# Kernel tuning notes

Hardware: AMD Instinct MI355X
Metric: run time of the kernel (lower is better)

The kernel has to match this reference:

```python
import jax, jax.numpy as jnp
import numpy as np

KW = 3          # kernel_width
PAD = (KW - 1) // 2


def setup_inputs() -> dict:
    key = jax.random.key(0)
    ks = jax.random.split(key, 7)
    B, QL, KL, QS, KS = 16, 1024, 1024, 512, 512
    q = jax.random.normal(ks[0], (B, QL, QS), dtype=jnp.float32)
    k = jax.random.normal(ks[1], (B, KL, KS), dtype=jnp.float32)
    # torch Linear weights: [out_features, in_features]
    Wk = jax.random.normal(ks[2], (KS * KW, QS), dtype=jnp.float32) * (1.0 / np.sqrt(QS))
    bk = jax.random.normal(ks[3], (KS * KW,), dtype=jnp.float32) * 0.02
    Wb = jax.random.normal(ks[4], (1, QS), dtype=jnp.float32) * (1.0 / np.sqrt(QS))
    bb = jax.random.normal(ks[5], (1,), dtype=jnp.float32) * 0.02
    bias_b = jax.random.normal(ks[6], (1,), dtype=jnp.float32)
    return {"q": q, "k": k, "Wk": Wk, "bk": bk, "Wb": Wb, "bb": bb, "bias_b": bias_b}


def reference(q, k, Wk, bk, Wb, bb, bias_b):
    B, QL, QS = q.shape
    _, KL, KS = k.shape
    # per-query dynamic kernels: [B, QL, KS, KW]
    kernel = (jnp.einsum('biq,oq->bio', q, Wk) + bk).reshape(B, QL, KS, KW)
    # per-query scalar bias: [B, QL]
    bias = (jnp.einsum('biq,oq->bio', q, Wb) + bb)[..., 0]
    # banded multiply-accumulate, equivalent to grouped conv1d with groups=B
    k_pad = jnp.pad(k, ((0, 0), (PAD, PAD), (0, 0)))  # [B, KL+KW-1, KS]
    # windows[b, j, t, c] = k_pad[b, j+t, c]  -> [B, KL, KW, KS]
    windows = jnp.stack([k_pad[:, t:t + KL, :] for t in range(KW)], axis=2)
    scores = jnp.einsum('bict,bjtc->bij', kernel, windows)
    return scores + bias[:, :, None] + bias_b[0]
```

## Files before the change

kernel.cpp:

```cpp
#include <hip/hip_runtime.h>

typedef unsigned short ushort_t;
typedef unsigned int uint32;
typedef __bf16 bf16x8 __attribute__((ext_vector_type(8)));
typedef float f32x4 __attribute__((ext_vector_type(4)));
typedef float f4 __attribute__((ext_vector_type(4)));
typedef unsigned short us4 __attribute__((ext_vector_type(4)));


__device__ __forceinline__ ushort_t f2bf(float f) {
    uint32 u = __builtin_bit_cast(uint32, f);
    u = (u + 0x7fffu + ((u >> 16) & 1u)) >> 16;
    return (ushort_t)u;
}

#define FULL_BAR() do { __builtin_amdgcn_sched_barrier(0); __builtin_amdgcn_s_barrier(); __builtin_amdgcn_sched_barrier(0); } while (0)
#define HALF_BAR() do { __builtin_amdgcn_sched_barrier(0); __builtin_amdgcn_s_barrier(); } while (0)

__global__ __launch_bounds__(256) void prep_q(const float* __restrict__ q,
                                              const float* __restrict__ Wb,
                                              const float* __restrict__ bb,
                                              ushort_t* __restrict__ qb,
                                              float* __restrict__ biasw) {
    const int tid = threadIdx.x;
    const int lane = tid & 63, wid = tid >> 6;
    const int m = blockIdx.x * 4 + wid;
    const float* qrow = q + (size_t)m * 512;

    f4 v0 = *(const f4*)(qrow + lane * 4);
    f4 v1 = *(const f4*)(qrow + 256 + lane * 4);
    f4 w0 = *(const f4*)(Wb + lane * 4);
    f4 w1 = *(const f4*)(Wb + 256 + lane * 4);

    float dot = v0[0]*w0[0] + v0[1]*w0[1] + v0[2]*w0[2] + v0[3]*w0[3]
              + v1[0]*w1[0] + v1[1]*w1[1] + v1[2]*w1[2] + v1[3]*w1[3];

    us4 o0, o1;
    o0[0]=f2bf(v0[0]); o0[1]=f2bf(v0[1]); o0[2]=f2bf(v0[2]); o0[3]=f2bf(v0[3]);
    o1[0]=f2bf(v1[0]); o1[1]=f2bf(v1[1]); o1[2]=f2bf(v1[2]); o1[3]=f2bf(v1[3]);
    *(us4*)(qb + (size_t)m * 512 + lane * 4) = o0;
    *(us4*)(qb + (size_t)m * 512 + 256 + lane * 4) = o1;

    #pragma unroll
    for (int off = 32; off >= 1; off >>= 1) dot += __shfl_xor(dot, off);
    if (lane == 0) biasw[m] = dot + bb[0];
}

__global__ __launch_bounds__(256) void prep_k(const float* __restrict__ k,
                                              const float* __restrict__ Wk,
                                              const float* __restrict__ bk,
                                              ushort_t* __restrict__ kbp,
                                              ushort_t* __restrict__ wkb,
                                              float* __restrict__ bkp) {
    const int gid = blockIdx.x * 256 + threadIdx.x;
    if (gid < 1536) bkp[gid] = bk[(gid & 511) * 3 + (gid >> 9)];

    const int KG = (16 * 1024 * 512) / 4;
    const int PG = (16 * 2 * 512) / 4;

    if (gid < KG) {
        const int e = gid * 4;
        const int b = e >> 19;
        const int rem = e & ((1 << 19) - 1);
        const int row = rem >> 9, c = rem & 511;
        f4 v = *(const f4*)(k + e);
        us4 o; o[0]=f2bf(v[0]); o[1]=f2bf(v[1]); o[2]=f2bf(v[2]); o[3]=f2bf(v[3]);
        *(us4*)(kbp + ((size_t)b * 1026 + row + 1) * 512 + c) = o;
    } else if (gid < KG + PG) {
        const int p = gid - KG;
        const int b = p >> 8, off = p & 255;
        const int row = (off < 128) ? 0 : 1025;
        const int c = (off & 127) * 4;
        us4 z; z[0]=0; z[1]=0; z[2]=0; z[3]=0;
        *(us4*)(kbp + ((size_t)b * 1026 + row) * 512 + c) = z;
    } else {
        const int w = gid - KG - PG;
        const int n = w >> 7;
        const int c = (w & 127) * 4;
        const int o = (n & 511) * 3 + (n >> 9);
        f4 v = *(const f4*)(Wk + (size_t)o * 512 + c);
        us4 ov; ov[0]=f2bf(v[0]); ov[1]=f2bf(v[1]); ov[2]=f2bf(v[2]); ov[3]=f2bf(v[3]);
        *(us4*)(wkb + (size_t)n * 512 + c) = ov;
    }
}


__device__ __forceinline__ void stage16k(const char* base, int ld, char* dst, int tid) {
    #pragma unroll
    for (int inst = 0; inst < 2; ++inst) {
        const int idx = inst * 512 + tid;
        const int srow = idx >> 2;
        const int scol = ((idx & 3) ^ ((idx >> 3) & 3)) << 4;
        __builtin_amdgcn_global_load_lds(
            (const __attribute__((address_space(1))) void*)(base + (size_t)srow * (size_t)ld + scol),
            (__attribute__((address_space(3))) void*)(dst + (inst * 512 + (tid & ~63)) * 16),
            16, 0, 0);
    }
}

__global__ __launch_bounds__(512) void gemm1(const ushort_t* __restrict__ qb,
                                             const ushort_t* __restrict__ wkb,
                                             const float* __restrict__ bkp,
                                             ushort_t* __restrict__ coef) {
    __shared__ alignas(16) char lds[65536];
    const int tid = threadIdx.x;
    const int l = tid & 63, wid = tid >> 6;
    const int wr = wid >> 2, wc = wid & 3;
    int bid = blockIdx.x;
    bid = (bid & 7) * 48 + (bid >> 3);
    const int mt = bid & 63, nt = bid >> 6;
    const int mbase = mt * 256, nbase = nt * 256;

    const char* Ag = (const char*)(qb + (size_t)mbase * 512);
    const char* Bg = (const char*)(wkb + (size_t)nbase * 512);
    const int NT = 16;

    const int r15 = l & 15, q = l >> 4;
    const int laneoff = r15 * 64 + (((q ^ (r15 >> 1)) & 3) << 4);
    const int wrA = wr * 8192 + laneoff;
    const int wcB = wc * 4096 + laneoff;

    f32x4 acc[8][4];
    #pragma unroll
    for (int mi = 0; mi < 8; ++mi)
        #pragma unroll
        for (int ni = 0; ni < 4; ++ni)
            #pragma unroll
            for (int r = 0; r < 4; ++r) acc[mi][ni][r] = 0.f;

    stage16k(Ag, 1024, lds, tid);
    stage16k(Bg, 1024, lds + 16384, tid);
    stage16k(Ag + 64, 1024, lds + 32768, tid);
    asm volatile("s_waitcnt vmcnt(2)" ::: "memory");
    FULL_BAR();

    for (int t = 0; t < NT; ++t) {
        const int cur = (t & 1) << 15;
        const int nxt = cur ^ 32768;
        const char* lA = lds + cur;
        const char* lB = lds + cur + 16384;
        const int tn1 = (t + 1 < NT) ? t + 1 : NT - 1;
        const int tn2 = (t + 2 < NT) ? t + 2 : NT - 1;

        bf16x8 a[8], b0, b1;
        #pragma unroll
        for (int mi = 0; mi < 8; ++mi) a[mi] = *(const bf16x8*)(lA + wrA + mi * 1024);
        b0 = *(const bf16x8*)(lB + wcB);
        b1 = *(const bf16x8*)(lB + wcB + 1024);
        stage16k(Bg + tn1 * 64, 1024, lds + nxt + 16384, tid);
        FULL_BAR();
        __builtin_amdgcn_s_setprio(1);
        #pragma unroll
        for (int mi = 0; mi < 8; ++mi) {
            acc[mi][0] = __builtin_amdgcn_mfma_f32_16x16x32_bf16(a[mi], b0, acc[mi][0], 0, 0, 0);
            acc[mi][1] = __builtin_amdgcn_mfma_f32_16x16x32_bf16(a[mi], b1, acc[mi][1], 0, 0, 0);
        }
        __builtin_amdgcn_s_setprio(0);
        HALF_BAR();
        b0 = *(const bf16x8*)(lB + wcB + 2048);
        b1 = *(const bf16x8*)(lB + wcB + 3072);
        stage16k(Ag + tn2 * 64, 1024, lds + cur, tid);
        asm volatile("s_waitcnt vmcnt(2)" ::: "memory");
        FULL_BAR();
        __builtin_amdgcn_s_setprio(1);
        #pragma unroll
        for (int mi = 0; mi < 8; ++mi) {
            acc[mi][2] = __builtin_amdgcn_mfma_f32_16x16x32_bf16(a[mi], b0, acc[mi][2], 0, 0, 0);
            acc[mi][3] = __builtin_amdgcn_mfma_f32_16x16x32_bf16(a[mi], b1, acc[mi][3], 0, 0, 0);
        }
        __builtin_amdgcn_s_setprio(0);
        HALF_BAR();
    }

    #pragma unroll
    for (int ni = 0; ni < 4; ++ni) {
        const int ncol = nbase + wc * 64 + ni * 16 + r15;
        const float bkv = bkp[ncol];
        #pragma unroll
        for (int mi = 0; mi < 8; ++mi) {
            const int mrow0 = mbase + wr * 128 + mi * 16 + q * 4;
            #pragma unroll
            for (int r = 0; r < 4; ++r)
                coef[(size_t)(mrow0 + r) * 1536 + ncol] = f2bf(acc[mi][ni][r] + bkv);
        }
    }
}

__global__ __launch_bounds__(512) void gemm2(const ushort_t* __restrict__ coef,
                                             const ushort_t* __restrict__ kbp,
                                             const float* __restrict__ biasw,
                                             const float* __restrict__ bias_b,
                                             float* __restrict__ out) {
    __shared__ alignas(16) char lds[65536];
    const int tid = threadIdx.x;
    const int l = tid & 63, wid = tid >> 6;
    const int wr = wid >> 2, wc = wid & 3;
    int bid = blockIdx.x;
    bid = (bid & 7) * 32 + (bid >> 3);
    const int jt = bid & 3, it = (bid >> 2) & 3, b = bid >> 4;
    const int ibase = it * 256, jbase = jt * 256;

    const char* Ag = (const char*)(coef + ((size_t)b * 1024 + ibase) * 1536);
    const char* Bg = (const char*)(kbp + ((size_t)b * 1026 + jbase) * 512);
    const int NT = 48;

    const int r15 = l & 15, q = l >> 4;
    const int laneoff = r15 * 64 + (((q ^ (r15 >> 1)) & 3) << 4);
    const int wrA = wr * 8192 + laneoff;
    const int wcB = wc * 4096 + laneoff;

    f32x4 acc[8][4];
    #pragma unroll
    for (int mi = 0; mi < 8; ++mi)
        #pragma unroll
        for (int ni = 0; ni < 4; ++ni)
            #pragma unroll
            for (int r = 0; r < 4; ++r) acc[mi][ni][r] = 0.f;

    stage16k(Ag, 3072, lds, tid);
    stage16k(Bg, 1024, lds + 16384, tid);
    stage16k(Ag + 64, 3072, lds + 32768, tid);
    asm volatile("s_waitcnt vmcnt(2)" ::: "memory");
    FULL_BAR();

    for (int t = 0; t < NT; ++t) {
        const int cur = (t & 1) << 15;
        const int nxt = cur ^ 32768;
        const char* lA = lds + cur;
        const char* lB = lds + cur + 16384;
        const int tn1 = (t + 1 < NT) ? t + 1 : NT - 1;
        const int tn2 = (t + 2 < NT) ? t + 2 : NT - 1;

        bf16x8 a[8], b0, b1;
        #pragma unroll
        for (int mi = 0; mi < 8; ++mi) a[mi] = *(const bf16x8*)(lA + wrA + mi * 1024);
        b0 = *(const bf16x8*)(lB + wcB);
        b1 = *(const bf16x8*)(lB + wcB + 1024);
        stage16k(Bg + (tn1 >> 4) * 1024 + (tn1 & 15) * 64, 1024, lds + nxt + 16384, tid);
        FULL_BAR();
        __builtin_amdgcn_s_setprio(1);
        #pragma unroll
        for (int mi = 0; mi < 8; ++mi) {
            acc[mi][0] = __builtin_amdgcn_mfma_f32_16x16x32_bf16(a[mi], b0, acc[mi][0], 0, 0, 0);
            acc[mi][1] = __builtin_amdgcn_mfma_f32_16x16x32_bf16(a[mi], b1, acc[mi][1], 0, 0, 0);
        }
        __builtin_amdgcn_s_setprio(0);
        HALF_BAR();
        b0 = *(const bf16x8*)(lB + wcB + 2048);
        b1 = *(const bf16x8*)(lB + wcB + 3072);
        stage16k(Ag + tn2 * 64, 3072, lds + cur, tid);
        asm volatile("s_waitcnt vmcnt(2)" ::: "memory");
        FULL_BAR();
        __builtin_amdgcn_s_setprio(1);
        #pragma unroll
        for (int mi = 0; mi < 8; ++mi) {
            acc[mi][2] = __builtin_amdgcn_mfma_f32_16x16x32_bf16(a[mi], b0, acc[mi][2], 0, 0, 0);
            acc[mi][3] = __builtin_amdgcn_mfma_f32_16x16x32_bf16(a[mi], b1, acc[mi][3], 0, 0, 0);
        }
        __builtin_amdgcn_s_setprio(0);
        HALF_BAR();
    }

    const float bb0v = bias_b[0];
    #pragma unroll
    for (int mi = 0; mi < 8; ++mi) {
        const int irow0 = ibase + wr * 128 + mi * 16 + q * 4;
        #pragma unroll
        for (int r = 0; r < 4; ++r) {
            const float bv = biasw[b * 1024 + irow0 + r] + bb0v;
            #pragma unroll
            for (int ni = 0; ni < 4; ++ni) {
                const int jcol = jbase + wc * 64 + ni * 16 + r15;
                out[((size_t)b << 20) + (size_t)(irow0 + r) * 1024 + jcol] = acc[mi][ni][r] + bv;
            }
        }
    }
}

extern "C" void kernel_launch(void* const* d_in, const int* in_sizes, int n_in,
                              void* d_out, int out_size, void* d_ws, size_t ws_size,
                              hipStream_t stream) {
    const float* q      = (const float*)d_in[0];
    const float* k      = (const float*)d_in[1];
    const float* Wk     = (const float*)d_in[2];
    const float* bk     = (const float*)d_in[3];
    const float* Wb     = (const float*)d_in[4];
    const float* bb     = (const float*)d_in[5];
    const float* bias_b = (const float*)d_in[6];
    float* out = (float*)d_out;

    ushort_t* ws   = (ushort_t*)d_ws;
    ushort_t* qb   = ws;
    ushort_t* kbp  = qb  + (size_t)16384 * 512;
    ushort_t* wkb  = kbp + (size_t)16 * 1026 * 512;
    ushort_t* coef = wkb + (size_t)1536 * 512;
    float*    biasw = (float*)(coef + (size_t)16384 * 1536);
    float*    bkp   = biasw + 16384;

    prep_q<<<4096, 256, 0, stream>>>(q, Wb, bb, qb, biasw);
    prep_k<<<8976, 256, 0, stream>>>(k, Wk, bk, kbp, wkb, bkp);
    gemm1<<<384, 512, 0, stream>>>(qb, wkb, bkp, coef);
    gemm2<<<256, 512, 0, stream>>>(coef, kbp, biasw, bias_b, out);
}
```

Before: 227.6 us.

## Deepen GEMM pipeline to 4-stage LDS ring and merge prep kernels

Both GEMM kernels move from a 2-buffer LDS scheme to a 4-slot ring (128 KB LDS) that prefetches three k-tiles ahead, and split the MFMA work by M halves instead of N halves. Waits become vmcnt(8), so more global loads stay in flight to hide memory latency. The two preprocessing kernels are merged into one launch with a block-index branch, removing one launch and its tail. The larger LDS footprint limits occupancy to one block per CU, and the extra prefetches add register pressure.

```diff
diff --git a/kernel.cpp b/kernel.cpp
--- a/kernel.cpp
+++ b/kernel.cpp
@@ -17,42 +17,43 @@
 #define FULL_BAR() do { __builtin_amdgcn_sched_barrier(0); __builtin_amdgcn_s_barrier(); __builtin_amdgcn_sched_barrier(0); } while (0)
 #define HALF_BAR() do { __builtin_amdgcn_sched_barrier(0); __builtin_amdgcn_s_barrier(); } while (0)
 
-__global__ __launch_bounds__(256) void prep_q(const float* __restrict__ q,
-                                              const float* __restrict__ Wb,
-                                              const float* __restrict__ bb,
-                                              ushort_t* __restrict__ qb,
-                                              float* __restrict__ biasw) {
+__global__ __launch_bounds__(256) void prep_all(const float* __restrict__ q,
+                                                const float* __restrict__ Wb,
+                                                const float* __restrict__ bb,
+                                                const float* __restrict__ k,
+                                                const float* __restrict__ Wk,
+                                                const float* __restrict__ bk,
+                                                ushort_t* __restrict__ qb,
+                                                float* __restrict__ biasw,
+                                                ushort_t* __restrict__ kbp,
+                                                ushort_t* __restrict__ wkb,
+                                                float* __restrict__ bkp) {
     const int tid = threadIdx.x;
-    const int lane = tid & 63, wid = tid >> 6;
-    const int m = blockIdx.x * 4 + wid;
-    const float* qrow = q + (size_t)m * 512;
-
-    f4 v0 = *(const f4*)(qrow + lane * 4);
-    f4 v1 = *(const f4*)(qrow + 256 + lane * 4);
-    f4 w0 = *(const f4*)(Wb + lane * 4);
-    f4 w1 = *(const f4*)(Wb + 256 + lane * 4);
-
-    float dot = v0[0]*w0[0] + v0[1]*w0[1] + v0[2]*w0[2] + v0[3]*w0[3]
-              + v1[0]*w1[0] + v1[1]*w1[1] + v1[2]*w1[2] + v1[3]*w1[3];
-
-    us4 o0, o1;
-    o0[0]=f2bf(v0[0]); o0[1]=f2bf(v0[1]); o0[2]=f2bf(v0[2]); o0[3]=f2bf(v0[3]);
-    o1[0]=f2bf(v1[0]); o1[1]=f2bf(v1[1]); o1[2]=f2bf(v1[2]); o1[3]=f2bf(v1[3]);
-    *(us4*)(qb + (size_t)m * 512 + lane * 4) = o0;
-    *(us4*)(qb + (size_t)m * 512 + 256 + lane * 4) = o1;
-
-    #pragma unroll
-    for (int off = 32; off >= 1; off >>= 1) dot += __shfl_xor(dot, off);
-    if (lane == 0) biasw[m] = dot + bb[0];
-}
-
-__global__ __launch_bounds__(256) void prep_k(const float* __restrict__ k,
-                                              const float* __restrict__ Wk,
-                                              const float* __restrict__ bk,
-                                              ushort_t* __restrict__ kbp,
-                                              ushort_t* __restrict__ wkb,
-                                              float* __restrict__ bkp) {
-    const int gid = blockIdx.x * 256 + threadIdx.x;
+    if (blockIdx.x < 4096) {
+        const int lane = tid & 63, wid = tid >> 6;
+        const int m = blockIdx.x * 4 + wid;
+        const float* qrow = q + (size_t)m * 512;
+
+        f4 v0 = *(const f4*)(qrow + lane * 4);
+        f4 v1 = *(const f4*)(qrow + 256 + lane * 4);
+        f4 w0 = *(const f4*)(Wb + lane * 4);
+        f4 w1 = *(const f4*)(Wb + 256 + lane * 4);
+
+        float dot = v0[0]*w0[0] + v0[1]*w0[1] + v0[2]*w0[2] + v0[3]*w0[3]
+                  + v1[0]*w1[0] + v1[1]*w1[1] + v1[2]*w1[2] + v1[3]*w1[3];
+
+        us4 o0, o1;
+        o0[0]=f2bf(v0[0]); o0[1]=f2bf(v0[1]); o0[2]=f2bf(v0[2]); o0[3]=f2bf(v0[3]);
+        o1[0]=f2bf(v1[0]); o1[1]=f2bf(v1[1]); o1[2]=f2bf(v1[2]); o1[3]=f2bf(v1[3]);
+        *(us4*)(qb + (size_t)m * 512 + lane * 4) = o0;
+        *(us4*)(qb + (size_t)m * 512 + 256 + lane * 4) = o1;
+
+        #pragma unroll
+        for (int off = 32; off >= 1; off >>= 1) dot += __shfl_xor(dot, off);
+        if (lane == 0) biasw[m] = dot + bb[0];
+        return;
+    }
+    const int gid = (blockIdx.x - 4096) * 256 + tid;
     if (gid < 1536) bkp[gid] = bk[(gid & 511) * 3 + (gid >> 9)];
 
     const int KG = (16 * 1024 * 512) / 4;
@@ -98,11 +99,60 @@
     }
 }
 
+#define GEMM_CORE(NT, A_OFF, B_OFF, A_LD, B_LD)                                            \
+    stage16k(Ag + (size_t)(A_OFF(0)), A_LD, lds, tid);                                     \
+    stage16k(Bg + (size_t)(B_OFF(0)), B_LD, lds + 16384, tid);                             \
+    stage16k(Ag + (size_t)(A_OFF(1)), A_LD, lds + 32768, tid);                             \
+    stage16k(Bg + (size_t)(B_OFF(1)), B_LD, lds + 32768 + 16384, tid);                     \
+    stage16k(Ag + (size_t)(A_OFF(2)), A_LD, lds + 65536, tid);                             \
+    stage16k(Bg + (size_t)(B_OFF(2)), B_LD, lds + 65536 + 16384, tid);                     \
+    asm volatile("s_waitcnt vmcnt(8)" ::: "memory");                                       \
+    FULL_BAR();                                                                            \
+    for (int t = 0; t < NT; ++t) {                                                         \
+        const char* lA = lds + ((t & 3) << 15);                                            \
+        const char* lB = lA + 16384;                                                       \
+        char* nb = lds + (((t + 3) & 3) << 15);                                            \
+        const int tn3 = (t + 3 < NT) ? t + 3 : NT - 1;                                     \
+        bf16x8 a[4], a2[4], b[4];                                                          \
+        _Pragma("unroll")                                                                  \
+        for (int mi = 0; mi < 4; ++mi) a[mi] = *(const bf16x8*)(lA + wrA + mi * 1024);     \
+        _Pragma("unroll")                                                                  \
+        for (int ni = 0; ni < 4; ++ni) b[ni] = *(const bf16x8*)(lB + wcB + ni * 1024);     \
+        stage16k(Ag + (size_t)(A_OFF(tn3)), A_LD, nb, tid);                                \
+        FULL_BAR();                                                                        \
+        __builtin_amdgcn_s_setprio(1);                                                     \
+        _Pragma("unroll")                                                                  \
+        for (int mi = 0; mi < 4; ++mi)                                                     \
+            _Pragma("unroll")                                                              \
+            for (int ni = 0; ni < 4; ++ni)                                                 \
+                acc[mi][ni] = __builtin_amdgcn_mfma_f32_16x16x32_bf16(a[mi], b[ni], acc[mi][ni], 0, 0, 0); \
+        __builtin_amdgcn_s_setprio(0);                                                     \
+        HALF_BAR();                                                                        \
+        _Pragma("unroll")                                                                  \
+        for (int mi = 0; mi < 4; ++mi) a2[mi] = *(const bf16x8*)(lA + wrA + (4 + mi) * 1024); \
+        stage16k(Bg + (size_t)(B_OFF(tn3)), B_LD, nb + 16384, tid);                        \
+        asm volatile("s_waitcnt vmcnt(8)" ::: "memory");                                   \
+        FULL_BAR();                                                                        \
+        __builtin_amdgcn_s_setprio(1);                                                     \
+        _Pragma("unroll")                                                                  \
+        for (int mi = 0; mi < 4; ++mi)                                                     \
+            _Pragma("unroll")                                                              \
+            for (int ni = 0; ni < 4; ++ni)                                                 \
+                acc[4 + mi][ni] = __builtin_amdgcn_mfma_f32_16x16x32_bf16(a2[mi], b[ni], acc[4 + mi][ni], 0, 0, 0); \
+        __builtin_amdgcn_s_setprio(0);                                                     \
+        HALF_BAR();                                                                        \
+    }
+
+#define A1OFF(tt) ((tt) * 64)
+#define B1OFF(tt) ((tt) * 64)
+#define A2OFF(tt) ((tt) * 64)
+#define B2OFF(tt) (((tt) >> 4) * 1024 + ((tt) & 15) * 64)
+
 __global__ __launch_bounds__(512) void gemm1(const ushort_t* __restrict__ qb,
                                              const ushort_t* __restrict__ wkb,
                                              const float* __restrict__ bkp,
                                              ushort_t* __restrict__ coef) {
-    __shared__ alignas(16) char lds[65536];
+    __shared__ alignas(16) char lds[131072];
     const int tid = threadIdx.x;
     const int l = tid & 63, wid = tid >> 6;
     const int wr = wid >> 2, wc = wid & 3;
@@ -113,7 +163,6 @@
 
     const char* Ag = (const char*)(qb + (size_t)mbase * 512);
     const char* Bg = (const char*)(wkb + (size_t)nbase * 512);
-    const int NT = 16;
 
     const int r15 = l & 15, q = l >> 4;
     const int laneoff = r15 * 64 + (((q ^ (r15 >> 1)) & 3) << 4);
@@ -128,49 +177,7 @@
             #pragma unroll
             for (int r = 0; r < 4; ++r) acc[mi][ni][r] = 0.f;
 
-    stage16k(Ag, 1024, lds, tid);
-    stage16k(Bg, 1024, lds + 16384, tid);
-    stage16k(Ag + 64, 1024, lds + 32768, tid);
-    asm volatile("s_waitcnt vmcnt(2)" ::: "memory");
-    FULL_BAR();
-
-    for (int t = 0; t < NT; ++t) {
-        const int cur = (t & 1) << 15;
-        const int nxt = cur ^ 32768;
-        const char* lA = lds + cur;
-        const char* lB = lds + cur + 16384;
-        const int tn1 = (t + 1 < NT) ? t + 1 : NT - 1;
-        const int tn2 = (t + 2 < NT) ? t + 2 : NT - 1;
-
-        bf16x8 a[8], b0, b1;
-        #pragma unroll
-        for (int mi = 0; mi < 8; ++mi) a[mi] = *(const bf16x8*)(lA + wrA + mi * 1024);
-        b0 = *(const bf16x8*)(lB + wcB);
-        b1 = *(const bf16x8*)(lB + wcB + 1024);
-        stage16k(Bg + tn1 * 64, 1024, lds + nxt + 16384, tid);
-        FULL_BAR();
-        __builtin_amdgcn_s_setprio(1);
-        #pragma unroll
-        for (int mi = 0; mi < 8; ++mi) {
-            acc[mi][0] = __builtin_amdgcn_mfma_f32_16x16x32_bf16(a[mi], b0, acc[mi][0], 0, 0, 0);
-            acc[mi][1] = __builtin_amdgcn_mfma_f32_16x16x32_bf16(a[mi], b1, acc[mi][1], 0, 0, 0);
-        }
-        __builtin_amdgcn_s_setprio(0);
-        HALF_BAR();
-        b0 = *(const bf16x8*)(lB + wcB + 2048);
-        b1 = *(const bf16x8*)(lB + wcB + 3072);
-        stage16k(Ag + tn2 * 64, 1024, lds + cur, tid);
-        asm volatile("s_waitcnt vmcnt(2)" ::: "memory");
-        FULL_BAR();
-        __builtin_amdgcn_s_setprio(1);
-        #pragma unroll
-        for (int mi = 0; mi < 8; ++mi) {
-            acc[mi][2] = __builtin_amdgcn_mfma_f32_16x16x32_bf16(a[mi], b0, acc[mi][2], 0, 0, 0);
-            acc[mi][3] = __builtin_amdgcn_mfma_f32_16x16x32_bf16(a[mi], b1, acc[mi][3], 0, 0, 0);
-        }
-        __builtin_amdgcn_s_setprio(0);
-        HALF_BAR();
-    }
+    GEMM_CORE(16, A1OFF, B1OFF, 1024, 1024)
 
     #pragma unroll
     for (int ni = 0; ni < 4; ++ni) {
@@ -191,7 +198,7 @@
                                              const float* __restrict__ biasw,
                                              const float* __restrict__ bias_b,
                                              float* __restrict__ out) {
-    __shared__ alignas(16) char lds[65536];
+    __shared__ alignas(16) char lds[131072];
     const int tid = threadIdx.x;
     const int l = tid & 63, wid = tid >> 6;
     const int wr = wid >> 2, wc = wid & 3;
@@ -202,7 +209,6 @@
 
     const char* Ag = (const char*)(coef + ((size_t)b * 1024 + ibase) * 1536);
     const char* Bg = (const char*)(kbp + ((size_t)b * 1026 + jbase) * 512);
-    const int NT = 48;
 
     const int r15 = l & 15, q = l >> 4;
     const int laneoff = r15 * 64 + (((q ^ (r15 >> 1)) & 3) << 4);
@@ -217,49 +223,7 @@
             #pragma unroll
             for (int r = 0; r < 4; ++r) acc[mi][ni][r] = 0.f;
 
-    stage16k(Ag, 3072, lds, tid);
-    stage16k(Bg, 1024, lds + 16384, tid);
-    stage16k(Ag + 64, 3072, lds + 32768, tid);
-    asm volatile("s_waitcnt vmcnt(2)" ::: "memory");
-    FULL_BAR();
-
-    for (int t = 0; t < NT; ++t) {
-        const int cur = (t & 1) << 15;
-        const int nxt = cur ^ 32768;
-        const char* lA = lds + cur;
-        const char* lB = lds + cur + 16384;
-        const int tn1 = (t + 1 < NT) ? t + 1 : NT - 1;
-        const int tn2 = (t + 2 < NT) ? t + 2 : NT - 1;
-
-        bf16x8 a[8], b0, b1;
-        #pragma unroll
-        for (int mi = 0; mi < 8; ++mi) a[mi] = *(const bf16x8*)(lA + wrA + mi * 1024);
-        b0 = *(const bf16x8*)(lB + wcB);
-        b1 = *(const bf16x8*)(lB + wcB + 1024);
-        stage16k(Bg + (tn1 >> 4) * 1024 + (tn1 & 15) * 64, 1024, lds + nxt + 16384, tid);
-        FULL_BAR();
-        __builtin_amdgcn_s_setprio(1);
-        #pragma unroll
-        for (int mi = 0; mi < 8; ++mi) {
-            acc[mi][0] = __builtin_amdgcn_mfma_f32_16x16x32_bf16(a[mi], b0, acc[mi][0], 0, 0, 0);
-            acc[mi][1] = __builtin_amdgcn_mfma_f32_16x16x32_bf16(a[mi], b1, acc[mi][1], 0, 0, 0);
-        }
-        __builtin_amdgcn_s_setprio(0);
-        HALF_BAR();
-        b0 = *(const bf16x8*)(lB + wcB + 2048);
-        b1 = *(const bf16x8*)(lB + wcB + 3072);
-        stage16k(Ag + tn2 * 64, 3072, lds + cur, tid);
-        asm volatile("s_waitcnt vmcnt(2)" ::: "memory");
-        FULL_BAR();
-        __builtin_amdgcn_s_setprio(1);
-        #pragma unroll
-        for (int mi = 0; mi < 8; ++mi) {
-            acc[mi][2] = __builtin_amdgcn_mfma_f32_16x16x32_bf16(a[mi], b0, acc[mi][2], 0, 0, 0);
-            acc[mi][3] = __builtin_amdgcn_mfma_f32_16x16x32_bf16(a[mi], b1, acc[mi][3], 0, 0, 0);
-        }
-        __builtin_amdgcn_s_setprio(0);
-        HALF_BAR();
-    }
+    GEMM_CORE(48, A2OFF, B2OFF, 3072, 1024)
 
     const float bb0v = bias_b[0];
     #pragma unroll
@@ -297,8 +261,7 @@
     float*    biasw = (float*)(coef + (size_t)16384 * 1536);
     float*    bkp   = biasw + 16384;
 
-    prep_q<<<4096, 256, 0, stream>>>(q, Wb, bb, qb, biasw);
-    prep_k<<<8976, 256, 0, stream>>>(k, Wk, bk, kbp, wkb, bkp);
+    prep_all<<<13072, 256, 0, stream>>>(q, Wb, bb, k, Wk, bk, qb, biasw, kbp, wkb, bkp);
     gemm1<<<384, 512, 0, stream>>>(qb, wkb, bkp, coef);
     gemm2<<<256, 512, 0, stream>>>(coef, kbp, biasw, bias_b, out);
 }
```

Result: no change. 226.7 us (-0.4%).
